# Performance work log

Measured on AMD Instinct MI355X. Metric: run time of the kernel, lower is better.

The kernel has to match this reference:

```python
import jax, jax.numpy as jnp
import numpy as np

B, D, H, E, K, A = 65536, 44, 256, 4, 2, 8  # batch, state_dim, hidden, experts, top_k, action_dim


def setup_inputs() -> dict:
    key = jax.random.key(0)
    ks = jax.random.split(key, 10)
    s = 0.1  # weight scale
    return dict(
        state=jax.random.normal(ks[0], (B, D), dtype=jnp.float32),
        rW1=jax.random.normal(ks[1], (D, H // 2)) * s, rb1=jnp.zeros((H // 2,)),
        rW2=jax.random.normal(ks[2], (H // 2, E)) * s, rb2=jnp.zeros((E,)),
        eW1=jax.random.normal(ks[3], (E, D, H)) * s, eb1=jnp.zeros((E, H)),
        eg1=jnp.ones((E, H)), ebt1=jnp.zeros((E, H)),
        eW2=jax.random.normal(ks[4], (E, H, H)) * s, eb2=jnp.zeros((E, H)),
        eg2=jnp.ones((E, H)), ebt2=jnp.zeros((E, H)),
        eW3=jax.random.normal(ks[5], (E, H, 2 * A)) * s, eb3=jnp.zeros((E, 2 * A)),
        vW1=jax.random.normal(ks[6], (D, H)) * s, vb1=jnp.zeros((H,)),
        vg=jnp.ones((H,)), vbt=jnp.zeros((H,)),
        vW2=jax.random.normal(ks[7], (H, H // 2)) * s, vb2=jnp.zeros((H // 2,)),
        vW3=jax.random.normal(ks[8], (H // 2, 1)) * s, vb3=jnp.zeros((1,)),
    )


def _ln(x, g, b):
    m = jnp.mean(x, axis=-1, keepdims=True)
    v = jnp.mean(jnp.square(x - m), axis=-1, keepdims=True)
    return (x - m) * jax.lax.rsqrt(v + 1e-5) * g + b


def reference(state, rW1, rb1, rW2, rb2,
              eW1, eb1, eg1, ebt1, eW2, eb2, eg2, ebt2, eW3, eb3,
              vW1, vb1, vg, vbt, vW2, vb2, vW3, vb3):
    # Router (eval mode: no noise)
    h = jax.nn.relu(state @ rW1 + rb1)
    router_probs = jax.nn.softmax(h @ rW2 + rb2, axis=-1)          # [B, E]
    top_v, top_i = jax.lax.top_k(router_probs, K)                  # [B, K]
    top_v = top_v / (jnp.sum(top_v, axis=-1, keepdims=True) + 1e-8)
    # Dense combine weights per expert (equivalent to per-sample gather/scatter loop)
    combine = jnp.sum(jax.nn.one_hot(top_i, E, dtype=state.dtype) * top_v[..., None], axis=1)  # [B, E]

    def expert(W1, b1, g1, bt1, W2, b2, g2, bt2, W3, b3):
        y = jax.nn.relu(_ln(state @ W1 + b1, g1, bt1))   # [B, H]
        y = jax.nn.relu(_ln(y @ W2 + b2, g2, bt2))       # [B, H]
        return y @ W3 + b3                               # [B, 2A]

    eout = jax.vmap(expert)(eW1, eb1, eg1, ebt1, eW2, eb2, eg2, ebt2, eW3, eb3)  # [E, B, 2A]
    mix = jnp.einsum('ebd,be->bd', eout, combine)        # [B, 2A]

    alpha = jax.nn.softplus(mix[:, :A]) + 1.0
    beta = jax.nn.softplus(mix[:, A:]) + 1.0

    v = jax.nn.relu(_ln(state @ vW1 + vb1, vg, vbt))
    v = jax.nn.relu(v @ vW2 + vb2)
    value = v @ vW3 + vb3                                # [B, 1]
    return alpha, beta, value, router_probs
```

## Files before the change

### kernel.cpp

```cpp
#include <hip/hip_runtime.h>
#include <math.h>

#define NB 65536

using f32x4 = __attribute__((ext_vector_type(4))) float;
using bf16x8 = __attribute__((ext_vector_type(8))) __bf16;

__device__ __forceinline__ unsigned short bfu(float x) {
    return __builtin_bit_cast(unsigned short, (__bf16)x);
}
__device__ __forceinline__ unsigned pk2(float lo, float hi) {
    return (unsigned)__builtin_bit_cast(unsigned short, (__bf16)lo)
         | ((unsigned)__builtin_bit_cast(unsigned short, (__bf16)hi) << 16);
}
__device__ __forceinline__ float softplus_f(float x) {
    return fmaxf(x, 0.f) + log1pf(expf(-fabsf(x)));
}

#define MFMA16(acc, a, b) acc = __builtin_amdgcn_mfma_f32_16x16x32_bf16(a, b, acc, 0, 0, 0)

__device__ __forceinline__ bf16x8 cvt8(f32x4 a, f32x4 b) {
    union { bf16x8 v; unsigned u[4]; } r;
    r.u[0] = pk2(a[0], a[1]); r.u[1] = pk2(a[2], a[3]);
    r.u[2] = pk2(b[0], b[1]); r.u[3] = pk2(b[2], b[3]);
    return r.v;
}

__device__ __forceinline__ const bf16x8* ys_frag(const unsigned short* ys, int row, int col) {
    return (const bf16x8*)&ys[row * 256 + (col ^ ((row & 7) << 3))];
}

__device__ __forceinline__ void ln_relu_store(
    f32x4* acc, const float* bs, const float* gs, const float* ts,
    unsigned int* ysu, int stripe, int g, int c)
{
    #pragma unroll
    for (int t = 0; t < 16; ++t) {
        float bb = bs[t * 16 + c];
        #pragma unroll
        for (int r = 0; r < 4; ++r) acc[t][r] += bb;
    }
    float sum[4] = {0.f, 0.f, 0.f, 0.f}, sq[4] = {0.f, 0.f, 0.f, 0.f};
    #pragma unroll
    for (int t = 0; t < 16; ++t) {
        #pragma unroll
        for (int r = 0; r < 4; ++r) { sum[r] += acc[t][r]; sq[r] += acc[t][r] * acc[t][r]; }
    }
    #pragma unroll
    for (int m = 1; m < 16; m <<= 1) {
        #pragma unroll
        for (int r = 0; r < 4; ++r) { sum[r] += __shfl_xor(sum[r], m); sq[r] += __shfl_xor(sq[r], m); }
    }
    float rs[4], nm[4];
    #pragma unroll
    for (int r = 0; r < 4; ++r) {
        float mean = sum[r] * (1.f / 256.f);
        float var = sq[r] * (1.f / 256.f) - mean * mean;
        rs[r] = rsqrtf(var + 1e-5f);
        nm[r] = -mean * rs[r];
    }
    const int odd = c & 1;
    const int ra = stripe + g * 4 + (odd ? 2 : 0);
    const int sza = (ra & 7) << 2, szb = ((ra + 1) & 7) << 2;
    #pragma unroll
    for (int t = 0; t < 16; ++t) {
        float gg = gs[t * 16 + c], bb = ts[t * 16 + c];
        float v0 = fmaxf(fmaf(fmaf(acc[t][0], rs[0], nm[0]), gg, bb), 0.f);
        float v1 = fmaxf(fmaf(fmaf(acc[t][1], rs[1], nm[1]), gg, bb), 0.f);
        float v2 = fmaxf(fmaf(fmaf(acc[t][2], rs[2], nm[2]), gg, bb), 0.f);
        float v3 = fmaxf(fmaf(fmaf(acc[t][3], rs[3], nm[3]), gg, bb), 0.f);
        float o0 = __shfl_xor(v0, 1), o1 = __shfl_xor(v1, 1);
        float o2 = __shfl_xor(v2, 1), o3 = __shfl_xor(v3, 1);
        unsigned p0 = pk2(odd ? o0 : v0, odd ? v0 : o0);
        unsigned p1 = pk2(odd ? o1 : v1, odd ? v1 : o1);
        unsigned p2 = pk2(odd ? o2 : v2, odd ? v2 : o2);
        unsigned p3 = pk2(odd ? o3 : v3, odd ? v3 : o3);
        unsigned pa = odd ? p2 : p0;
        unsigned pb = odd ? p3 : p1;
        int cp = t * 8 + (c >> 1);
        ysu[ra * 128 + (cp ^ sza)] = pa;
        ysu[(ra + 1) * 128 + (cp ^ szb)] = pb;
    }
}

__global__ __launch_bounds__(256) void k1_prep_router(
    const float* __restrict__ state,
    const float* __restrict__ rW1, const float* __restrict__ rb1,
    const float* __restrict__ rW2, const float* __restrict__ rb2,
    const float* __restrict__ eW1, const float* __restrict__ eW2, const float* __restrict__ eW3,
    const float* __restrict__ vW1, const float* __restrict__ vW2,
    unsigned int* __restrict__ w1c, unsigned int* __restrict__ vw1c,
    unsigned int* __restrict__ w2c, unsigned int* __restrict__ vw2c,
    unsigned short* __restrict__ w3t,
    float* __restrict__ out_probs, float* __restrict__ combine)
{
    const int blk = blockIdx.x;
    if (blk < 45) {
        int id = blk * 256 + threadIdx.x;
        if (id < 1024) {
            int e = id >> 8, h = id & 255;
            for (int ch = 0; ch < 2; ++ch)
                #pragma unroll
                for (int d2 = 0; d2 < 16; ++d2) {
                    int k = ch * 32 + d2 * 2;
                    float x0 = (k < 44) ? eW1[(e * 44 + k) * 256 + h] : 0.f;
                    float x1 = (k + 1 < 44) ? eW1[(e * 44 + k + 1) * 256 + h] : 0.f;
                    w1c[((e * 2 + ch) * 256 + h) * 16 + d2] = pk2(x0, x1);
                }
        } else if (id < 1280) {
            int h = id - 1024;
            for (int ch = 0; ch < 2; ++ch)
                #pragma unroll
                for (int d2 = 0; d2 < 16; ++d2) {
                    int k = ch * 32 + d2 * 2;
                    float x0 = (k < 44) ? vW1[k * 256 + h] : 0.f;
                    float x1 = (k + 1 < 44) ? vW1[(k + 1) * 256 + h] : 0.f;
                    vw1c[(ch * 256 + h) * 16 + d2] = pk2(x0, x1);
                }
        } else if (id < 9472) {
            int t = id - 1280;
            int e = t >> 11, ch = (t >> 8) & 7, hout = t & 255;
            const float* base = eW2 + (size_t)e * 65536 + hout;
            #pragma unroll
            for (int d2 = 0; d2 < 16; ++d2) {
                int k = ch * 32 + d2 * 2;
                w2c[((e * 8 + ch) * 256 + hout) * 16 + d2] = pk2(base[k * 256], base[(k + 1) * 256]);
            }
        } else if (id < 10496) {
            int t = id - 9472;
            int ch = t >> 7, hout = t & 127;
            #pragma unroll
            for (int d2 = 0; d2 < 16; ++d2) {
                int k = ch * 32 + d2 * 2;
                vw2c[(ch * 128 + hout) * 16 + d2] = pk2(vW2[k * 128 + hout], vW2[(k + 1) * 128 + hout]);
            }
        } else if (id < 11520) {
            int t = id - 10496;
            int kc = t & 15, eo = t >> 4;
            int e = eo >> 4, o = eo & 15;
            #pragma unroll
            for (int i = 0; i < 16; ++i) {
                int k = kc * 16 + i;
                w3t[eo * 256 + k] = bfu(eW3[(size_t)e * 4096 + k * 16 + o]);
            }
        }
        return;
    }

    int b = (blk - 45) * 256 + threadIdx.x;
    float s[44];
    const float* sp = state + (size_t)b * 44;
    #pragma unroll
    for (int d = 0; d < 44; ++d) s[d] = sp[d];

    float l0 = rb2[0], l1 = rb2[1], l2 = rb2[2], l3 = rb2[3];
    for (int j4 = 0; j4 < 32; ++j4) {
        f32x4 h = *(const f32x4*)&rb1[j4 * 4];
        #pragma unroll
        for (int d = 0; d < 44; ++d) {
            f32x4 w = *(const f32x4*)&rW1[d * 128 + j4 * 4];
            h += s[d] * w;
        }
        #pragma unroll
        for (int jj = 0; jj < 4; ++jj) {
            float hv = fmaxf(h[jj], 0.f);
            f32x4 w2 = *(const f32x4*)&rW2[(j4 * 4 + jj) * 4];
            l0 += hv * w2[0]; l1 += hv * w2[1]; l2 += hv * w2[2]; l3 += hv * w2[3];
        }
    }
    float mx = fmaxf(fmaxf(l0, l1), fmaxf(l2, l3));
    float e0 = expf(l0 - mx), e1 = expf(l1 - mx), e2 = expf(l2 - mx), e3 = expf(l3 - mx);
    float inv = 1.f / (e0 + e1 + e2 + e3);
    float p0 = e0 * inv, p1 = e1 * inv, p2 = e2 * inv, p3 = e3 * inv;
    f32x4 probs = {p0, p1, p2, p3};
    *(f32x4*)&out_probs[(size_t)b * 4] = probs;

    int i1 = 0; float v1 = p0;
    if (p1 > v1) { v1 = p1; i1 = 1; }
    if (p2 > v1) { v1 = p2; i1 = 2; }
    if (p3 > v1) { v1 = p3; i1 = 3; }
    int i2 = -1; float v2 = -1.f;
    if (i1 != 0 && p0 > v2) { v2 = p0; i2 = 0; }
    if (i1 != 1 && p1 > v2) { v2 = p1; i2 = 1; }
    if (i1 != 2 && p2 > v2) { v2 = p2; i2 = 2; }
    if (i1 != 3 && p3 > v2) { v2 = p3; i2 = 3; }
    float cn = 1.f / (v1 + v2 + 1e-8f);
    float c1 = v1 * cn, c2 = v2 * cn;
    f32x4 cm;
    cm[0] = (i1 == 0) ? c1 : (i2 == 0) ? c2 : 0.f;
    cm[1] = (i1 == 1) ? c1 : (i2 == 1) ? c2 : 0.f;
    cm[2] = (i1 == 2) ? c1 : (i2 == 2) ? c2 : 0.f;
    cm[3] = (i1 == 3) ? c1 : (i2 == 3) ? c2 : 0.f;
    *(f32x4*)&combine[(size_t)b * 4] = cm;
}

#define SM_YS    0
#define SM_WBUF  32768
#define SM_W3S   53248
#define SM_B1    61696
#define SM_G1    62720
#define SM_T1    63744
#define SM_B2    64768
#define SM_G2    65792
#define SM_T2    66816
#define SM_B3    67840
#define SM_CMB   67904
#define SM_TOTAL 68928

__global__ __launch_bounds__(256, 2) void k2_experts_value(
    const float* __restrict__ state,
    const float* __restrict__ eb1, const float* __restrict__ eg1, const float* __restrict__ ebt1,
    const float* __restrict__ eb2, const float* __restrict__ eg2, const float* __restrict__ ebt2,
    const float* __restrict__ eb3,
    const float* __restrict__ vb1, const float* __restrict__ vg, const float* __restrict__ vbt,
    const float* __restrict__ vb2, const float* __restrict__ vW3, const float* __restrict__ vb3,
    const f32x4* __restrict__ w1c, const f32x4* __restrict__ w2c,
    const f32x4* __restrict__ vw1c, const f32x4* __restrict__ vw2c,
    const f32x4* __restrict__ w3tv,
    const float* __restrict__ combine,
    float* __restrict__ out_alpha, float* __restrict__ out_beta, float* __restrict__ out_value)
{
    __shared__ __align__(16) unsigned char smem[SM_TOTAL];
    unsigned short* ys = (unsigned short*)(smem + SM_YS);
    unsigned int* ysu = (unsigned int*)(smem + SM_YS);
    unsigned short* wbuf = (unsigned short*)(smem + SM_WBUF);
    unsigned short* w3s = (unsigned short*)(smem + SM_W3S);
    float* b1s = (float*)(smem + SM_B1);
    float* g1s = (float*)(smem + SM_G1);
    float* t1s = (float*)(smem + SM_T1);
    float* b2s = (float*)(smem + SM_B2);
    float* g2s = (float*)(smem + SM_G2);
    float* t2s = (float*)(smem + SM_T2);
    float* b3s = (float*)(smem + SM_B3);
    float* cmbs = (float*)(smem + SM_CMB);

    const int tid = threadIdx.x;
    const int wid = tid >> 6;
    const int lane = tid & 63;
    const int c = lane & 15;
    const int g = lane >> 4;
    const int stripe = wid * 16;
    const bool is_expert = (blockIdx.x < 1024);
    const int brow = (is_expert ? blockIdx.x : (blockIdx.x - 1024)) * 64;

    bf16x8 a1[2];
    {
        const float* srow = state + (size_t)(brow + stripe + c) * 44;
        f32x4 v0 = *(const f32x4*)(srow + g * 8);
        f32x4 v1 = *(const f32x4*)(srow + g * 8 + 4);
        a1[0] = cvt8(v0, v1);
        f32x4 z = {0.f, 0.f, 0.f, 0.f};
        f32x4 w0 = z, w1 = z;
        if (g == 0) { w0 = *(const f32x4*)(srow + 32); w1 = *(const f32x4*)(srow + 36); }
        else if (g == 1) { w0 = *(const f32x4*)(srow + 40); }
        a1[1] = cvt8(w0, w1);
    }

    f32x4 st[4];

    if (is_expert) {
        cmbs[tid] = combine[(size_t)brow * 4 + tid];
        float mix0 = 0.f, mix1 = 0.f, mix2 = 0.f, mix3 = 0.f;

        for (int e = 0; e < 4; ++e) {
            #pragma unroll
            for (int j = 0; j < 4; ++j) st[j] = w1c[(e * 2) * 1024 + tid + j * 256];
            f32x4 s3a = w3tv[e * 512 + tid];
            f32x4 s3b = w3tv[e * 512 + tid + 256];
            float rb1v = eb1[e * 256 + tid], rg1v = eg1[e * 256 + tid], rt1v = ebt1[e * 256 + tid];
            float rb2v = eb2[e * 256 + tid], rg2v = eg2[e * 256 + tid], rt2v = ebt2[e * 256 + tid];
            float b3v = (tid < 16) ? eb3[e * 16 + tid] : 0.f;
            __syncthreads();
            #pragma unroll
            for (int j = 0; j < 4; ++j) {
                int u = tid + j * 256;
                *(f32x4*)&wbuf[(u >> 2) * 40 + (u & 3) * 8] = st[j];
            }
            *(f32x4*)&w3s[(tid >> 5) * 264 + (tid & 31) * 8] = s3a;
            { int u2 = tid + 256; *(f32x4*)&w3s[(u2 >> 5) * 264 + (u2 & 31) * 8] = s3b; }
            b1s[tid] = rb1v; g1s[tid] = rg1v; t1s[tid] = rt1v;
            b2s[tid] = rb2v; g2s[tid] = rg2v; t2s[tid] = rt2v;
            if (tid < 16) b3s[tid] = b3v;
            __syncthreads();

            f32x4 acc1[16];
            #pragma unroll
            for (int t = 0; t < 16; ++t) acc1[t] = (f32x4){0.f, 0.f, 0.f, 0.f};
            #pragma unroll
            for (int t = 0; t < 16; ++t) {
                bf16x8 bfr = *(const bf16x8*)&wbuf[(t * 16 + c) * 40 + g * 8];
                MFMA16(acc1[t], a1[0], bfr);
            }
            #pragma unroll
            for (int j = 0; j < 4; ++j) st[j] = w1c[(e * 2 + 1) * 1024 + tid + j * 256];
            __syncthreads();
            #pragma unroll
            for (int j = 0; j < 4; ++j) {
                int u = tid + j * 256;
                *(f32x4*)&wbuf[(u >> 2) * 40 + (u & 3) * 8] = st[j];
            }
            __syncthreads();
            #pragma unroll
            for (int t = 0; t < 16; ++t) {
                bf16x8 bfr = *(const bf16x8*)&wbuf[(t * 16 + c) * 40 + g * 8];
                MFMA16(acc1[t], a1[1], bfr);
            }
            ln_relu_store(acc1, b1s, g1s, t1s, ysu, stripe, g, c);

            f32x4 acc2[16];
            #pragma unroll
            for (int t = 0; t < 16; ++t) acc2[t] = (f32x4){0.f, 0.f, 0.f, 0.f};
            for (int ch = 0; ch < 8; ++ch) {
                #pragma unroll
                for (int j = 0; j < 4; ++j) st[j] = w2c[(e * 8 + ch) * 1024 + tid + j * 256];
                __syncthreads();
                #pragma unroll
                for (int j = 0; j < 4; ++j) {
                    int u = tid + j * 256;
                    *(f32x4*)&wbuf[(u >> 2) * 40 + (u & 3) * 8] = st[j];
                }
                __syncthreads();
                bf16x8 a = *ys_frag(ys, stripe + c, ch * 32 + g * 8);
                #pragma unroll
                for (int t = 0; t < 16; ++t) {
                    bf16x8 bfr = *(const bf16x8*)&wbuf[(t * 16 + c) * 40 + g * 8];
                    MFMA16(acc2[t], a, bfr);
                }
            }
            ln_relu_store(acc2, b2s, g2s, t2s, ysu, stripe, g, c);

            f32x4 acc3 = (f32x4){0.f, 0.f, 0.f, 0.f};
            #pragma unroll
            for (int s = 0; s < 8; ++s) {
                bf16x8 a = *ys_frag(ys, stripe + c, s * 32 + g * 8);
                bf16x8 bfr = *(const bf16x8*)&w3s[c * 264 + s * 32 + g * 8];
                MFMA16(acc3, a, bfr);
            }
            float bb3 = b3s[c];
            mix0 += cmbs[(stripe + g * 4 + 0) * 4 + e] * (acc3[0] + bb3);
            mix1 += cmbs[(stripe + g * 4 + 1) * 4 + e] * (acc3[1] + bb3);
            mix2 += cmbs[(stripe + g * 4 + 2) * 4 + e] * (acc3[2] + bb3);
            mix3 += cmbs[(stripe + g * 4 + 3) * 4 + e] * (acc3[3] + bb3);
        }

        int row0 = brow + stripe + g * 4;
        float sp0 = softplus_f(mix0) + 1.f;
        float sp1 = softplus_f(mix1) + 1.f;
        float sp2 = softplus_f(mix2) + 1.f;
        float sp3 = softplus_f(mix3) + 1.f;
        if (c < 8) {
            out_alpha[(size_t)(row0 + 0) * 8 + c] = sp0;
            out_alpha[(size_t)(row0 + 1) * 8 + c] = sp1;
            out_alpha[(size_t)(row0 + 2) * 8 + c] = sp2;
            out_alpha[(size_t)(row0 + 3) * 8 + c] = sp3;
        } else {
            out_beta[(size_t)(row0 + 0) * 8 + (c - 8)] = sp0;
            out_beta[(size_t)(row0 + 1) * 8 + (c - 8)] = sp1;
            out_beta[(size_t)(row0 + 2) * 8 + (c - 8)] = sp2;
            out_beta[(size_t)(row0 + 3) * 8 + (c - 8)] = sp3;
        }
    } else {
        #pragma unroll
        for (int j = 0; j < 4; ++j) st[j] = vw1c[tid + j * 256];
        float rb1v = vb1[tid], rg1v = vg[tid], rt1v = vbt[tid];
        float b2v = (tid < 128) ? vb2[tid] : 0.f;
        float w3v = (tid < 128) ? vW3[tid] : 0.f;
        __syncthreads();
        #pragma unroll
        for (int j = 0; j < 4; ++j) {
            int u = tid + j * 256;
            *(f32x4*)&wbuf[(u >> 2) * 40 + (u & 3) * 8] = st[j];
        }
        b1s[tid] = rb1v; g1s[tid] = rg1v; t1s[tid] = rt1v;
        if (tid < 128) { b2s[tid] = b2v; g2s[tid] = w3v; }
        __syncthreads();

        f32x4 acc1[16];
        #pragma unroll
        for (int t = 0; t < 16; ++t) acc1[t] = (f32x4){0.f, 0.f, 0.f, 0.f};
        #pragma unroll
        for (int t = 0; t < 16; ++t) {
            bf16x8 bfr = *(const bf16x8*)&wbuf[(t * 16 + c) * 40 + g * 8];
            MFMA16(acc1[t], a1[0], bfr);
        }
        #pragma unroll
        for (int j = 0; j < 4; ++j) st[j] = vw1c[1024 + tid + j * 256];
        __syncthreads();
        #pragma unroll
        for (int j = 0; j < 4; ++j) {
            int u = tid + j * 256;
            *(f32x4*)&wbuf[(u >> 2) * 40 + (u & 3) * 8] = st[j];
        }
        __syncthreads();
        #pragma unroll
        for (int t = 0; t < 16; ++t) {
            bf16x8 bfr = *(const bf16x8*)&wbuf[(t * 16 + c) * 40 + g * 8];
            MFMA16(acc1[t], a1[1], bfr);
        }
        ln_relu_store(acc1, b1s, g1s, t1s, ysu, stripe, g, c);

        f32x4 acc2[8];
        #pragma unroll
        for (int t = 0; t < 8; ++t) acc2[t] = (f32x4){0.f, 0.f, 0.f, 0.f};
        for (int ch = 0; ch < 8; ++ch) {
            st[0] = vw2c[ch * 512 + tid];
            st[1] = vw2c[ch * 512 + tid + 256];
            __syncthreads();
            {
                int u = tid;
                *(f32x4*)&wbuf[(u >> 2) * 40 + (u & 3) * 8] = st[0];
                u = tid + 256;
                *(f32x4*)&wbuf[(u >> 2) * 40 + (u & 3) * 8] = st[1];
            }
            __syncthreads();
            bf16x8 a = *ys_frag(ys, stripe + c, ch * 32 + g * 8);
            #pragma unroll
            for (int t = 0; t < 8; ++t) {
                bf16x8 bfr = *(const bf16x8*)&wbuf[(t * 16 + c) * 40 + g * 8];
                MFMA16(acc2[t], a, bfr);
            }
        }

        float part[4] = {0.f, 0.f, 0.f, 0.f};
        #pragma unroll
        for (int t = 0; t < 8; ++t) {
            float bb = b2s[t * 16 + c], ww = g2s[t * 16 + c];
            #pragma unroll
            for (int r = 0; r < 4; ++r) part[r] += fmaxf(acc2[t][r] + bb, 0.f) * ww;
        }
        #pragma unroll
        for (int m = 1; m < 16; m <<= 1) {
            #pragma unroll
            for (int r = 0; r < 4; ++r) part[r] += __shfl_xor(part[r], m);
        }
        if (c == 0) {
            float v3 = vb3[0];
            int row = brow + stripe + g * 4;
            out_value[row + 0] = part[0] + v3;
            out_value[row + 1] = part[1] + v3;
            out_value[row + 2] = part[2] + v3;
            out_value[row + 3] = part[3] + v3;
        }
    }
}

extern "C" void kernel_launch(void* const* d_in, const int* in_sizes, int n_in,
                              void* d_out, int out_size, void* d_ws, size_t ws_size,
                              hipStream_t stream)
{
    const float* state = (const float*)d_in[0];
    const float* rW1  = (const float*)d_in[1];
    const float* rb1  = (const float*)d_in[2];
    const float* rW2  = (const float*)d_in[3];
    const float* rb2  = (const float*)d_in[4];
    const float* eW1  = (const float*)d_in[5];
    const float* eb1  = (const float*)d_in[6];
    const float* eg1  = (const float*)d_in[7];
    const float* ebt1 = (const float*)d_in[8];
    const float* eW2  = (const float*)d_in[9];
    const float* eb2  = (const float*)d_in[10];
    const float* eg2  = (const float*)d_in[11];
    const float* ebt2 = (const float*)d_in[12];
    const float* eW3  = (const float*)d_in[13];
    const float* eb3  = (const float*)d_in[14];
    const float* vW1  = (const float*)d_in[15];
    const float* vb1  = (const float*)d_in[16];
    const float* vg   = (const float*)d_in[17];
    const float* vbt  = (const float*)d_in[18];
    const float* vW2  = (const float*)d_in[19];
    const float* vb2  = (const float*)d_in[20];
    const float* vW3  = (const float*)d_in[21];
    const float* vb3  = (const float*)d_in[22];

    float* out = (float*)d_out;
    float* out_alpha = out;
    float* out_beta  = out + (size_t)NB * 8;
    float* out_value = out + (size_t)NB * 16;
    float* out_probs = out + (size_t)NB * 17;

    char* ws = (char*)d_ws;
    float* combine      = (float*)ws;
    unsigned int* w1c   = (unsigned int*)(ws + 0x100000);
    unsigned int* vw1c  = (unsigned int*)(ws + 0x120000);
    unsigned int* w2c   = (unsigned int*)(ws + 0x128000);
    unsigned int* vw2c  = (unsigned int*)(ws + 0x1A8000);
    unsigned short* w3t = (unsigned short*)(ws + 0x1B8000);

    hipLaunchKernelGGL(k1_prep_router, dim3(301), dim3(256), 0, stream,
                       state, rW1, rb1, rW2, rb2, eW1, eW2, eW3, vW1, vW2,
                       w1c, vw1c, w2c, vw2c, w3t, out_probs, combine);
    hipLaunchKernelGGL(k2_experts_value, dim3(2048), dim3(256), 0, stream,
                       state, eb1, eg1, ebt1, eb2, eg2, ebt2, eb3,
                       vb1, vg, vbt, vb2, vW3, vb3,
                       (const f32x4*)w1c, (const f32x4*)w2c,
                       (const f32x4*)vw1c, (const f32x4*)vw2c,
                       (const f32x4*)w3t,
                       combine, out_alpha, out_beta, out_value);
}
```

Before: 288.6 us.

## Double-buffer weight chunks in LDS and prelayout weights into MFMA fragment images

The prep kernel now writes every weight matrix as a fragment-ordered bf16 image, with one 16-byte store per thread, so the main kernel can copy chunks linearly into LDS without the padded-stride rearrangement. The main kernel ping-pongs between two LDS buffers: while one chunk is consumed by MFMAs, the next chunk is loaded from global memory and written to the other buffer. This halves the barriers per chunk and prefetches across stages and experts (W1 to W2 to W3 to the next expert's W1). The cost is more LDS per block (about 72 KB versus 69 KB) and more registers held for the prefetched chunk, which could pressure occupancy at two blocks per CU. The linear fragment layout may also cause LDS bank conflicts compared with the old 40-element padded stride.

Measured after the change: 279.0 us. -3.3%, faster.

```diff
diff --git a/kernel.cpp b/kernel.cpp
--- a/kernel.cpp
+++ b/kernel.cpp
@@ -4,11 +4,9 @@
 #define NB 65536
 
 using f32x4 = __attribute__((ext_vector_type(4))) float;
+using u32x4 = __attribute__((ext_vector_type(4))) unsigned;
 using bf16x8 = __attribute__((ext_vector_type(8))) __bf16;
 
-__device__ __forceinline__ unsigned short bfu(float x) {
-    return __builtin_bit_cast(unsigned short, (__bf16)x);
-}
 __device__ __forceinline__ unsigned pk2(float lo, float hi) {
     return (unsigned)__builtin_bit_cast(unsigned short, (__bf16)lo)
          | ((unsigned)__builtin_bit_cast(unsigned short, (__bf16)hi) << 16);
@@ -28,6 +26,26 @@
 
 __device__ __forceinline__ const bf16x8* ys_frag(const unsigned short* ys, int row, int col) {
     return (const bf16x8*)&ys[row * 256 + (col ^ ((row & 7) << 3))];
+}
+
+template<int NJ>
+__device__ __forceinline__ void ldch(f32x4* r, const f32x4* __restrict__ src, int tid) {
+    #pragma unroll
+    for (int j = 0; j < NJ; ++j) r[j] = src[tid + j * 256];
+}
+template<int NJ>
+__device__ __forceinline__ void wrch(unsigned short* buf, const f32x4* r, int tid) {
+    #pragma unroll
+    for (int j = 0; j < NJ; ++j) *(f32x4*)&buf[(size_t)(tid + j * 256) * 8] = r[j];
+}
+
+template<int NT>
+__device__ __forceinline__ void mfma_bcols(f32x4* acc, bf16x8 a, const unsigned short* bufp, int c, int g) {
+    #pragma unroll
+    for (int t = 0; t < NT; ++t) {
+        bf16x8 b = *(const bf16x8*)&bufp[t * 512 + g * 128 + c * 8];
+        MFMA16(acc[t], a, b);
+    }
 }
 
 __device__ __forceinline__ void ln_relu_store(
@@ -89,65 +107,71 @@
     const float* __restrict__ rW2, const float* __restrict__ rb2,
     const float* __restrict__ eW1, const float* __restrict__ eW2, const float* __restrict__ eW3,
     const float* __restrict__ vW1, const float* __restrict__ vW2,
-    unsigned int* __restrict__ w1c, unsigned int* __restrict__ vw1c,
-    unsigned int* __restrict__ w2c, unsigned int* __restrict__ vw2c,
-    unsigned short* __restrict__ w3t,
+    unsigned int* __restrict__ w1img, unsigned int* __restrict__ w2img,
+    unsigned int* __restrict__ vw1img, unsigned int* __restrict__ vw2img,
+    unsigned int* __restrict__ w3img,
     float* __restrict__ out_probs, float* __restrict__ combine)
 {
     const int blk = blockIdx.x;
-    if (blk < 45) {
-        int id = blk * 256 + threadIdx.x;
-        if (id < 1024) {
-            int e = id >> 8, h = id & 255;
-            for (int ch = 0; ch < 2; ++ch)
-                #pragma unroll
-                for (int d2 = 0; d2 < 16; ++d2) {
-                    int k = ch * 32 + d2 * 2;
-                    float x0 = (k < 44) ? eW1[(e * 44 + k) * 256 + h] : 0.f;
-                    float x1 = (k + 1 < 44) ? eW1[(e * 44 + k + 1) * 256 + h] : 0.f;
-                    w1c[((e * 2 + ch) * 256 + h) * 16 + d2] = pk2(x0, x1);
-                }
-        } else if (id < 1280) {
-            int h = id - 1024;
-            for (int ch = 0; ch < 2; ++ch)
-                #pragma unroll
-                for (int d2 = 0; d2 < 16; ++d2) {
-                    int k = ch * 32 + d2 * 2;
-                    float x0 = (k < 44) ? vW1[k * 256 + h] : 0.f;
-                    float x1 = (k + 1 < 44) ? vW1[(k + 1) * 256 + h] : 0.f;
-                    vw1c[(ch * 256 + h) * 16 + d2] = pk2(x0, x1);
-                }
-        } else if (id < 9472) {
-            int t = id - 1280;
-            int e = t >> 11, ch = (t >> 8) & 7, hout = t & 255;
-            const float* base = eW2 + (size_t)e * 65536 + hout;
-            #pragma unroll
-            for (int d2 = 0; d2 < 16; ++d2) {
-                int k = ch * 32 + d2 * 2;
-                w2c[((e * 8 + ch) * 256 + hout) * 16 + d2] = pk2(base[k * 256], base[(k + 1) * 256]);
+    if (blk < 192) {
+        int fid = blk * 256 + threadIdx.x;
+        float v[8];
+        unsigned int* dst;
+        if (fid < 8192) {
+            int e = fid >> 11, ch = (fid >> 10) & 1, rr = fid & 1023;
+            int t = rr >> 6, g = (rr >> 4) & 3, c = rr & 15;
+            int h = t * 16 + c, k0 = ch * 32 + g * 8;
+            #pragma unroll
+            for (int j = 0; j < 8; ++j) {
+                int k = k0 + j;
+                v[j] = (k < 44) ? eW1[(e * 44 + k) * 256 + h] : 0.f;
             }
-        } else if (id < 10496) {
-            int t = id - 9472;
-            int ch = t >> 7, hout = t & 127;
-            #pragma unroll
-            for (int d2 = 0; d2 < 16; ++d2) {
-                int k = ch * 32 + d2 * 2;
-                vw2c[(ch * 128 + hout) * 16 + d2] = pk2(vW2[k * 128 + hout], vW2[(k + 1) * 128 + hout]);
+            dst = w1img + (size_t)fid * 4;
+        } else if (fid < 40960) {
+            int f = fid - 8192;
+            int e = f >> 13, ch = (f >> 10) & 7, rr = f & 1023;
+            int t = rr >> 6, g = (rr >> 4) & 3, c = rr & 15;
+            int h = t * 16 + c, k0 = ch * 32 + g * 8;
+            const float* base = eW2 + (size_t)e * 65536 + h;
+            #pragma unroll
+            for (int j = 0; j < 8; ++j) v[j] = base[(size_t)(k0 + j) * 256];
+            dst = w2img + (size_t)f * 4;
+        } else if (fid < 43008) {
+            int f = fid - 40960;
+            int ch = f >> 10, rr = f & 1023;
+            int t = rr >> 6, g = (rr >> 4) & 3, c = rr & 15;
+            int h = t * 16 + c, k0 = ch * 32 + g * 8;
+            #pragma unroll
+            for (int j = 0; j < 8; ++j) {
+                int k = k0 + j;
+                v[j] = (k < 44) ? vW1[k * 256 + h] : 0.f;
             }
-        } else if (id < 11520) {
-            int t = id - 10496;
-            int kc = t & 15, eo = t >> 4;
-            int e = eo >> 4, o = eo & 15;
-            #pragma unroll
-            for (int i = 0; i < 16; ++i) {
-                int k = kc * 16 + i;
-                w3t[eo * 256 + k] = bfu(eW3[(size_t)e * 4096 + k * 16 + o]);
-            }
-        }
+            dst = vw1img + (size_t)f * 4;
+        } else if (fid < 47104) {
+            int f = fid - 43008;
+            int ch = f >> 9, rr = f & 511;
+            int t = rr >> 6, g = (rr >> 4) & 3, c = rr & 15;
+            int h = t * 16 + c, k0 = ch * 32 + g * 8;
+            #pragma unroll
+            for (int j = 0; j < 8; ++j) v[j] = vW2[(k0 + j) * 128 + h];
+            dst = vw2img + (size_t)f * 4;
+        } else {
+            int f = fid - 47104;
+            int e = f >> 9, rr = f & 511;
+            int s = rr >> 6, g = (rr >> 4) & 3, o = rr & 15;
+            int k0 = s * 32 + g * 8;
+            #pragma unroll
+            for (int j = 0; j < 8; ++j) v[j] = eW3[(size_t)e * 4096 + (k0 + j) * 16 + o];
+            dst = w3img + (size_t)f * 4;
+        }
+        u32x4 out;
+        #pragma unroll
+        for (int p = 0; p < 4; ++p) out[p] = pk2(v[2 * p], v[2 * p + 1]);
+        *(u32x4*)dst = out;
         return;
     }
 
-    int b = (blk - 45) * 256 + threadIdx.x;
+    int b = (blk - 192) * 256 + threadIdx.x;
     float s[44];
     const float* sp = state + (size_t)b * 44;
     #pragma unroll
@@ -195,17 +219,19 @@
 }
 
 #define SM_YS    0
-#define SM_WBUF  32768
-#define SM_W3S   53248
-#define SM_B1    61696
-#define SM_G1    62720
-#define SM_T1    63744
-#define SM_B2    64768
-#define SM_G2    65792
-#define SM_T2    66816
-#define SM_B3    67840
-#define SM_CMB   67904
-#define SM_TOTAL 68928
+#define SM_BUFA  32768
+#define SM_BUFB  49152
+#define SM_B1    65536
+#define SM_G1    66560
+#define SM_T1    67584
+#define SM_B2    68608
+#define SM_G2    69632
+#define SM_T2    70656
+#define SM_B3    71680
+#define SM_CMB   71744
+#define SM_TOTAL 72768
+
+#define SWAPBUF() { unsigned short* _t = cur; cur = nxt; nxt = _t; }
 
 __global__ __launch_bounds__(256, 2) void k2_experts_value(
     const float* __restrict__ state,
@@ -214,17 +240,15 @@
     const float* __restrict__ eb3,
     const float* __restrict__ vb1, const float* __restrict__ vg, const float* __restrict__ vbt,
     const float* __restrict__ vb2, const float* __restrict__ vW3, const float* __restrict__ vb3,
-    const f32x4* __restrict__ w1c, const f32x4* __restrict__ w2c,
-    const f32x4* __restrict__ vw1c, const f32x4* __restrict__ vw2c,
-    const f32x4* __restrict__ w3tv,
+    const f32x4* __restrict__ w1v, const f32x4* __restrict__ w2v,
+    const f32x4* __restrict__ vw1v, const f32x4* __restrict__ vw2v,
+    const f32x4* __restrict__ w3v,
     const float* __restrict__ combine,
     float* __restrict__ out_alpha, float* __restrict__ out_beta, float* __restrict__ out_value)
 {
     __shared__ __align__(16) unsigned char smem[SM_TOTAL];
     unsigned short* ys = (unsigned short*)(smem + SM_YS);
     unsigned int* ysu = (unsigned int*)(smem + SM_YS);
-    unsigned short* wbuf = (unsigned short*)(smem + SM_WBUF);
-    unsigned short* w3s = (unsigned short*)(smem + SM_W3S);
     float* b1s = (float*)(smem + SM_B1);
     float* g1s = (float*)(smem + SM_G1);
     float* t1s = (float*)(smem + SM_T1);
@@ -233,6 +257,8 @@
     float* t2s = (float*)(smem + SM_T2);
     float* b3s = (float*)(smem + SM_B3);
     float* cmbs = (float*)(smem + SM_CMB);
+    unsigned short* cur = (unsigned short*)(smem + SM_BUFA);
+    unsigned short* nxt = (unsigned short*)(smem + SM_BUFB);
 
     const int tid = threadIdx.x;
     const int wid = tid >> 6;
@@ -256,91 +282,78 @@
         a1[1] = cvt8(w0, w1);
     }
 
-    f32x4 st[4];
+    f32x4 r[4];
 
     if (is_expert) {
         cmbs[tid] = combine[(size_t)brow * 4 + tid];
         float mix0 = 0.f, mix1 = 0.f, mix2 = 0.f, mix3 = 0.f;
 
+        ldch<4>(r, w1v, tid);
+        wrch<4>(cur, r, tid);
+        ldch<4>(r, w1v + 1024, tid);
+        __syncthreads();
+
         for (int e = 0; e < 4; ++e) {
-            #pragma unroll
-            for (int j = 0; j < 4; ++j) st[j] = w1c[(e * 2) * 1024 + tid + j * 256];
-            f32x4 s3a = w3tv[e * 512 + tid];
-            f32x4 s3b = w3tv[e * 512 + tid + 256];
-            float rb1v = eb1[e * 256 + tid], rg1v = eg1[e * 256 + tid], rt1v = ebt1[e * 256 + tid];
-            float rb2v = eb2[e * 256 + tid], rg2v = eg2[e * 256 + tid], rt2v = ebt2[e * 256 + tid];
-            float b3v = (tid < 16) ? eb3[e * 16 + tid] : 0.f;
-            __syncthreads();
-            #pragma unroll
-            for (int j = 0; j < 4; ++j) {
-                int u = tid + j * 256;
-                *(f32x4*)&wbuf[(u >> 2) * 40 + (u & 3) * 8] = st[j];
+            const int en = (e < 3) ? e + 1 : 3;
+            float xb1 = eb1[e * 256 + tid], xg1 = eg1[e * 256 + tid], xt1 = ebt1[e * 256 + tid];
+            float xb2 = eb2[e * 256 + tid], xg2 = eg2[e * 256 + tid], xt2 = ebt2[e * 256 + tid];
+            b1s[tid] = xb1; g1s[tid] = xg1; t1s[tid] = xt1;
+            b2s[tid] = xb2; g2s[tid] = xg2; t2s[tid] = xt2;
+            if (tid < 16) b3s[tid] = eb3[e * 16 + tid];
+
+            f32x4 acc1[16];
+            #pragma unroll
+            for (int t = 0; t < 16; ++t) acc1[t] = (f32x4){0.f, 0.f, 0.f, 0.f};
+
+            wrch<4>(nxt, r, tid);
+            ldch<4>(r, w2v + (size_t)(e * 8 + 0) * 1024, tid);
+            mfma_bcols<16>(acc1, a1[0], cur, c, g);
+            __syncthreads(); SWAPBUF();
+
+            wrch<4>(nxt, r, tid);
+            ldch<4>(r, w2v + (size_t)(e * 8 + 1) * 1024, tid);
+            mfma_bcols<16>(acc1, a1[1], cur, c, g);
+            ln_relu_store(acc1, b1s, g1s, t1s, ysu, stripe, g, c);
+            __syncthreads(); SWAPBUF();
+
+            f32x4 acc2[16];
+            #pragma unroll
+            for (int t = 0; t < 16; ++t) acc2[t] = (f32x4){0.f, 0.f, 0.f, 0.f};
+
+            #pragma unroll
+            for (int ch = 0; ch < 7; ++ch) {
+                wrch<4>(nxt, r, tid);
+                if (ch < 6) ldch<4>(r, w2v + (size_t)(e * 8 + ch + 2) * 1024, tid);
+                else        ldch<2>(r, w3v + (size_t)e * 512, tid);
+                bf16x8 a = *ys_frag(ys, stripe + c, ch * 32 + g * 8);
+                mfma_bcols<16>(acc2, a, cur, c, g);
+                __syncthreads(); SWAPBUF();
             }
-            *(f32x4*)&w3s[(tid >> 5) * 264 + (tid & 31) * 8] = s3a;
-            { int u2 = tid + 256; *(f32x4*)&w3s[(u2 >> 5) * 264 + (u2 & 31) * 8] = s3b; }
-            b1s[tid] = rb1v; g1s[tid] = rg1v; t1s[tid] = rt1v;
-            b2s[tid] = rb2v; g2s[tid] = rg2v; t2s[tid] = rt2v;
-            if (tid < 16) b3s[tid] = b3v;
-            __syncthreads();
-
-            f32x4 acc1[16];
-            #pragma unroll
-            for (int t = 0; t < 16; ++t) acc1[t] = (f32x4){0.f, 0.f, 0.f, 0.f};
-            #pragma unroll
-            for (int t = 0; t < 16; ++t) {
-                bf16x8 bfr = *(const bf16x8*)&wbuf[(t * 16 + c) * 40 + g * 8];
-                MFMA16(acc1[t], a1[0], bfr);
-            }
-            #pragma unroll
-            for (int j = 0; j < 4; ++j) st[j] = w1c[(e * 2 + 1) * 1024 + tid + j * 256];
-            __syncthreads();
-            #pragma unroll
-            for (int j = 0; j < 4; ++j) {
-                int u = tid + j * 256;
-                *(f32x4*)&wbuf[(u >> 2) * 40 + (u & 3) * 8] = st[j];
-            }
-            __syncthreads();
-            #pragma unroll
-            for (int t = 0; t < 16; ++t) {
-                bf16x8 bfr = *(const bf16x8*)&wbuf[(t * 16 + c) * 40 + g * 8];
-                MFMA16(acc1[t], a1[1], bfr);
-            }
-            ln_relu_store(acc1, b1s, g1s, t1s, ysu, stripe, g, c);
-
-            f32x4 acc2[16];
-            #pragma unroll
-            for (int t = 0; t < 16; ++t) acc2[t] = (f32x4){0.f, 0.f, 0.f, 0.f};
-            for (int ch = 0; ch < 8; ++ch) {
-                #pragma unroll
-                for (int j = 0; j < 4; ++j) st[j] = w2c[(e * 8 + ch) * 1024 + tid + j * 256];
-                __syncthreads();
-                #pragma unroll
-                for (int j = 0; j < 4; ++j) {
-                    int u = tid + j * 256;
-                    *(f32x4*)&wbuf[(u >> 2) * 40 + (u & 3) * 8] = st[j];
-                }
-                __syncthreads();
-                bf16x8 a = *ys_frag(ys, stripe + c, ch * 32 + g * 8);
-                #pragma unroll
-                for (int t = 0; t < 16; ++t) {
-                    bf16x8 bfr = *(const bf16x8*)&wbuf[(t * 16 + c) * 40 + g * 8];
-                    MFMA16(acc2[t], a, bfr);
-                }
+
+            wrch<2>(nxt, r, tid);
+            ldch<4>(r, w1v + (size_t)(en * 2) * 1024, tid);
+            {
+                bf16x8 a = *ys_frag(ys, stripe + c, 7 * 32 + g * 8);
+                mfma_bcols<16>(acc2, a, cur, c, g);
             }
             ln_relu_store(acc2, b2s, g2s, t2s, ysu, stripe, g, c);
-
+            __syncthreads(); SWAPBUF();
+
+            wrch<4>(nxt, r, tid);
+            ldch<4>(r, w1v + (size_t)(en * 2 + 1) * 1024, tid);
             f32x4 acc3 = (f32x4){0.f, 0.f, 0.f, 0.f};
             #pragma unroll
             for (int s = 0; s < 8; ++s) {
                 bf16x8 a = *ys_frag(ys, stripe + c, s * 32 + g * 8);
-                bf16x8 bfr = *(const bf16x8*)&w3s[c * 264 + s * 32 + g * 8];
-                MFMA16(acc3, a, bfr);
+                bf16x8 b = *(const bf16x8*)&cur[s * 512 + g * 128 + c * 8];
+                MFMA16(acc3, a, b);
             }
             float bb3 = b3s[c];
             mix0 += cmbs[(stripe + g * 4 + 0) * 4 + e] * (acc3[0] + bb3);
             mix1 += cmbs[(stripe + g * 4 + 1) * 4 + e] * (acc3[1] + bb3);
             mix2 += cmbs[(stripe + g * 4 + 2) * 4 + e] * (acc3[2] + bb3);
             mix3 += cmbs[(stripe + g * 4 + 3) * 4 + e] * (acc3[3] + bb3);
+            __syncthreads(); SWAPBUF();
         }
 
         int row0 = brow + stripe + g * 4;
@@ -360,65 +373,44 @@
             out_beta[(size_t)(row0 + 3) * 8 + (c - 8)] = sp3;
         }
     } else {
-        #pragma unroll
-        for (int j = 0; j < 4; ++j) st[j] = vw1c[tid + j * 256];
-        float rb1v = vb1[tid], rg1v = vg[tid], rt1v = vbt[tid];
-        float b2v = (tid < 128) ? vb2[tid] : 0.f;
-        float w3v = (tid < 128) ? vW3[tid] : 0.f;
+        b1s[tid] = vb1[tid]; g1s[tid] = vg[tid]; t1s[tid] = vbt[tid];
+        if (tid < 128) { b2s[tid] = vb2[tid]; g2s[tid] = vW3[tid]; }
+
+        ldch<4>(r, vw1v, tid);
+        wrch<4>(cur, r, tid);
+        ldch<4>(r, vw1v + 1024, tid);
         __syncthreads();
-        #pragma unroll
-        for (int j = 0; j < 4; ++j) {
-            int u = tid + j * 256;
-            *(f32x4*)&wbuf[(u >> 2) * 40 + (u & 3) * 8] = st[j];
-        }
-        b1s[tid] = rb1v; g1s[tid] = rg1v; t1s[tid] = rt1v;
-        if (tid < 128) { b2s[tid] = b2v; g2s[tid] = w3v; }
-        __syncthreads();
 
         f32x4 acc1[16];
         #pragma unroll
         for (int t = 0; t < 16; ++t) acc1[t] = (f32x4){0.f, 0.f, 0.f, 0.f};
-        #pragma unroll
-        for (int t = 0; t < 16; ++t) {
-            bf16x8 bfr = *(const bf16x8*)&wbuf[(t * 16 + c) * 40 + g * 8];
-            MFMA16(acc1[t], a1[0], bfr);
-        }
-        #pragma unroll
-        for (int j = 0; j < 4; ++j) st[j] = vw1c[1024 + tid + j * 256];
-        __syncthreads();
-        #pragma unroll
-        for (int j = 0; j < 4; ++j) {
-            int u = tid + j * 256;
-            *(f32x4*)&wbuf[(u >> 2) * 40 + (u & 3) * 8] = st[j];
-        }
-        __syncthreads();
-        #pragma unroll
-        for (int t = 0; t < 16; ++t) {
-            bf16x8 bfr = *(const bf16x8*)&wbuf[(t * 16 + c) * 40 + g * 8];
-            MFMA16(acc1[t], a1[1], bfr);
-        }
+
+        wrch<4>(nxt, r, tid);
+        ldch<2>(r, vw2v, tid);
+        mfma_bcols<16>(acc1, a1[0], cur, c, g);
+        __syncthreads(); SWAPBUF();
+
+        wrch<4>(nxt, r, tid);
+        ldch<2>(r, vw2v + 512, tid);
+        mfma_bcols<16>(acc1, a1[1], cur, c, g);
         ln_relu_store(acc1, b1s, g1s, t1s, ysu, stripe, g, c);
+        __syncthreads(); SWAPBUF();
 
         f32x4 acc2[8];
         #pragma unroll
         for (int t = 0; t < 8; ++t) acc2[t] = (f32x4){0.f, 0.f, 0.f, 0.f};
-        for (int ch = 0; ch < 8; ++ch) {
-            st[0] = vw2c[ch * 512 + tid];
-            st[1] = vw2c[ch * 512 + tid + 256];
-            __syncthreads();
-            {
-                int u = tid;
-                *(f32x4*)&wbuf[(u >> 2) * 40 + (u & 3) * 8] = st[0];
-                u = tid + 256;
-                *(f32x4*)&wbuf[(u >> 2) * 40 + (u & 3) * 8] = st[1];
-            }
-            __syncthreads();
+
+        #pragma unroll
+        for (int ch = 0; ch < 7; ++ch) {
+            wrch<2>(nxt, r, tid);
+            if (ch < 6) ldch<2>(r, vw2v + (size_t)(ch + 2) * 512, tid);
             bf16x8 a = *ys_frag(ys, stripe + c, ch * 32 + g * 8);
-            #pragma unroll
-            for (int t = 0; t < 8; ++t) {
-                bf16x8 bfr = *(const bf16x8*)&wbuf[(t * 16 + c) * 40 + g * 8];
-                MFMA16(acc2[t], a, bfr);
-            }
+            mfma_bcols<8>(acc2, a, cur, c, g);
+            __syncthreads(); SWAPBUF();
+        }
+        {
+            bf16x8 a = *ys_frag(ys, stripe + c, 7 * 32 + g * 8);
+            mfma_bcols<8>(acc2, a, cur, c, g);
         }
 
         float part[4] = {0.f, 0.f, 0.f, 0.f};
@@ -426,12 +418,12 @@
         for (int t = 0; t < 8; ++t) {
             float bb = b2s[t * 16 + c], ww = g2s[t * 16 + c];
             #pragma unroll
-            for (int r = 0; r < 4; ++r) part[r] += fmaxf(acc2[t][r] + bb, 0.f) * ww;
+            for (int q = 0; q < 4; ++q) part[q] += fmaxf(acc2[t][q] + bb, 0.f) * ww;
         }
         #pragma unroll
         for (int m = 1; m < 16; m <<= 1) {
             #pragma unroll
-            for (int r = 0; r < 4; ++r) part[r] += __shfl_xor(part[r], m);
+            for (int q = 0; q < 4; ++q) part[q] += __shfl_xor(part[q], m);
         }
         if (c == 0) {
             float v3 = vb3[0];
@@ -479,21 +471,21 @@
     float* out_probs = out + (size_t)NB * 17;
 
     char* ws = (char*)d_ws;
-    float* combine      = (float*)ws;
-    unsigned int* w1c   = (unsigned int*)(ws + 0x100000);
-    unsigned int* vw1c  = (unsigned int*)(ws + 0x120000);
-    unsigned int* w2c   = (unsigned int*)(ws + 0x128000);
-    unsigned int* vw2c  = (unsigned int*)(ws + 0x1A8000);
-    unsigned short* w3t = (unsigned short*)(ws + 0x1B8000);
-
-    hipLaunchKernelGGL(k1_prep_router, dim3(301), dim3(256), 0, stream,
+    float* combine        = (float*)ws;
+    unsigned int* w1img   = (unsigned int*)(ws + 0x100000);
+    unsigned int* w2img   = (unsigned int*)(ws + 0x120000);
+    unsigned int* vw1img  = (unsigned int*)(ws + 0x1A0000);
+    unsigned int* vw2img  = (unsigned int*)(ws + 0x1A8000);
+    unsigned int* w3img   = (unsigned int*)(ws + 0x1B8000);
+
+    hipLaunchKernelGGL(k1_prep_router, dim3(448), dim3(256), 0, stream,
                        state, rW1, rb1, rW2, rb2, eW1, eW2, eW3, vW1, vW2,
-                       w1c, vw1c, w2c, vw2c, w3t, out_probs, combine);
+                       w1img, w2img, vw1img, vw2img, w3img, out_probs, combine);
     hipLaunchKernelGGL(k2_experts_value, dim3(2048), dim3(256), 0, stream,
                        state, eb1, eg1, ebt1, eb2, eg2, ebt2, eb3,
                        vb1, vg, vbt, vb2, vW3, vb3,
-                       (const f32x4*)w1c, (const f32x4*)w2c,
-                       (const f32x4*)vw1c, (const f32x4*)vw2c,
-                       (const f32x4*)w3t,
+                       (const f32x4*)w1img, (const f32x4*)w2img,
+                       (const f32x4*)vw1img, (const f32x4*)vw2img,
+                       (const f32x4*)w3img,
                        combine, out_alpha, out_beta, out_value);
 }
```
